# Performance work log

Hardware: AMD Instinct MI355X
Metric: run time of the kernel (lower is better)

Reference implementation:

```python
import jax, jax.numpy as jnp
import numpy as np

EPS = 1e-7  # keras.backend.epsilon()
ROUTINGS = 3


def squash(s, axis=-1):
    # standard capsule squash: ||s||^2/(1+||s||^2) * s/||s||
    n2 = jnp.sum(jnp.square(s), axis=axis, keepdims=True)
    return s * (n2 / (1.0 + n2)) / jnp.sqrt(n2 + EPS)


def setup_inputs() -> dict:
    key = jax.random.key(0)
    k1, k2 = jax.random.split(key)
    B, I, K = 32, 2048, 8          # batch, input capsules, input capsule dim
    J, D = 32, 16                  # output capsules (num_capsules), dim_capsules
    x = jax.random.normal(k1, (B, I, K), dtype=jnp.float32)
    # add_weight with random_normal_initializer(stddev=0.1), shape [J, I, D, K]
    W = 0.1 * jax.random.normal(k2, (J, I, D, K), dtype=jnp.float32)
    return {"x": x, "W": W}


def reference(x, W):
    # u_ji_hat[b,j,i,d] = sum_k W[j,i,d,k] * x[b,i,k]  (the map_fn batched matmul)
    u_hat = jnp.einsum('jidk,bik->bjid', W, x)  # [B, J, I, D]
    B, J, I, D = u_hat.shape
    b = jnp.zeros((B, J, I), dtype=u_hat.dtype)  # routing logits b_ij
    v = None
    for r in range(ROUTINGS):
        c = jax.nn.softmax(b, axis=1)                 # softmax over output capsules J
        s = jnp.einsum('bji,bjid->bjd', c, u_hat)     # weighted sum over input caps i
        v = squash(s, axis=-1)                        # squash over capsule dim (axis=-2 pre-squeeze)
        if r < ROUTINGS - 1:
            # agreement = u_hat^T v : sum over capsule dim d
            b = b + jnp.einsum('bjid,bjd->bji', u_hat, v)
    return v  # [B, J, D] == tf.squeeze(v_j, [2, 4])
```

## Files before the change

kernel.cpp:

```cpp
#include <hip/hip_runtime.h>
#include <hip/hip_fp16.h>


#define ICAP    2048
#define JD      512
#define S_ELEMS 16384
#define EPSQ    1e-7f
#define NBP     256
#define ICH     8

typedef _Float16 h2v __attribute__((ext_vector_type(2)));
union H8 { int4 i4; h2v h[4]; };

#if defined(__has_builtin) && __has_builtin(__builtin_amdgcn_fdot2)
#define FDOT2(a, b, c) __builtin_amdgcn_fdot2((a), (b), (c), false)
#else
__device__ inline float FDOT2(h2v a, h2v b, float c) {
    return c + (float)a[0] * (float)b[0] + (float)a[1] * (float)b[1];
}
#endif
#if defined(__has_builtin) && __has_builtin(__builtin_amdgcn_rcpf)
#define FAST_RCP(x) __builtin_amdgcn_rcpf(x)
#else
#define FAST_RCP(x) (1.0f / (x))
#endif
#if defined(__has_builtin) && __has_builtin(__builtin_amdgcn_rsqf)
#define FAST_RSQ(x) __builtin_amdgcn_rsqf(x)
#else
#define FAST_RSQ(x) rsqrtf(x)
#endif

__global__ __launch_bounds__(256)
void caps_prep(const float4* __restrict__ Wv, const float* __restrict__ x,
               ushort4* __restrict__ Wt, __half* __restrict__ xh) {
    const int i = blockIdx.x;
    const int t = threadIdx.x;
#pragma unroll
    for (int q = 0; q < 4; ++q) {
        const int f  = q * 256 + t;
        const int jj = f >> 5, c = f & 31;
        const float4 w = Wv[(size_t)jj * 65536 + (size_t)i * 32 + c];
        ushort4 h;
        h.x = __half_as_ushort(__float2half(w.x));
        h.y = __half_as_ushort(__float2half(w.y));
        h.z = __half_as_ushort(__float2half(w.z));
        h.w = __half_as_ushort(__float2half(w.w));
        const int dh = c >> 4, cc = (c & 15) >> 1, sub = c & 1;
        Wt[((size_t)i * 512 + cc * 64 + 2 * jj + dh) * 2 + sub] = h;
    }
    const int b = t >> 3, k = t & 7;
    const size_t xi = ((size_t)b * ICAP + i) * 8 + k;
    xh[xi] = __float2half(x[xi]);
}

template <int FIRST>
__global__ __launch_bounds__(512, 1)
void caps_pass(const int4* __restrict__ Wt, const int4* __restrict__ xh,
               const float* __restrict__ vsum, __half* __restrict__ partials) {
    const int tid  = threadIdx.x;
    const int wave = tid >> 6;
    const int lane = tid & 63;
    const int j    = lane & 31;
    const int dh   = lane >> 5;
    const int i0   = blockIdx.x * ICH;

    float vs[4][8], sacc[4][8];
#pragma unroll
    for (int bb = 0; bb < 4; ++bb) {
        const int b = wave + 8 * bb;
        if (!FIRST) {
            const float* vp = vsum + b * JD + j * 16 + dh * 8;
            const float4 a  = *reinterpret_cast<const float4*>(vp);
            const float4 bq = *reinterpret_cast<const float4*>(vp + 4);
            vs[bb][0]=a.x; vs[bb][1]=a.y; vs[bb][2]=a.z; vs[bb][3]=a.w;
            vs[bb][4]=bq.x; vs[bb][5]=bq.y; vs[bb][6]=bq.z; vs[bb][7]=bq.w;
        }
#pragma unroll
        for (int r = 0; r < 8; ++r) sacc[bb][r] = 0.f;
    }

    const int4* wp = Wt + (size_t)i0 * 512 + 2 * j + dh;

#pragma unroll
    for (int il = 0; il < ICH; ++il) {
        H8 w8[8];
#pragma unroll
        for (int cc = 0; cc < 8; ++cc)
            w8[cc].i4 = wp[(size_t)il * 512 + cc * 64];

        const int gi = i0 + il;
#pragma unroll
        for (int bb = 0; bb < 4; ++bb) {
            const int b = wave + 8 * bb;
            H8 xv;
            xv.i4 = xh[(size_t)b * ICAP + gi];

            float u[8], tpart = 0.f;
#pragma unroll
            for (int r = 0; r < 8; ++r) {
                float acc = FDOT2(w8[r].h[0], xv.h[0], 0.f);
                acc = FDOT2(w8[r].h[1], xv.h[1], acc);
                acc = FDOT2(w8[r].h[2], xv.h[2], acc);
                acc = FDOT2(w8[r].h[3], xv.h[3], acc);
                u[r] = acc;
                if (!FIRST) tpart = fmaf(acc, vs[bb][r], tpart);
            }
            float c;
            if (FIRST) {
                c = 0.03125f;
            } else {
                const float t = tpart + __shfl_xor(tpart, 32);
                const float e = __expf(t);
                float se = e;
#pragma unroll
                for (int off = 1; off <= 16; off <<= 1)
                    se += __shfl_xor(se, off);
                c = e * FAST_RCP(se);
            }
#pragma unroll
            for (int r = 0; r < 8; ++r)
                sacc[bb][r] = fmaf(c, u[r], sacc[bb][r]);
        }
    }

    __half* pout = partials + (size_t)blockIdx.x * S_ELEMS;
#pragma unroll
    for (int bb = 0; bb < 4; ++bb) {
        const int b = wave + 8 * bb;
        union { int4 v; __half2 h[4]; } pk;
#pragma unroll
        for (int r = 0; r < 4; ++r)
            pk.h[r] = __floats2half2_rn(sacc[bb][2 * r], sacc[bb][2 * r + 1]);
        *reinterpret_cast<int4*>(pout + b * JD + j * 16 + dh * 8) = pk.v;
    }
}

__global__ __launch_bounds__(1024)
void caps_reduce(const __half* __restrict__ partials, float* __restrict__ vsum,
                 float* __restrict__ out, int first) {
    __shared__ float buf[16][80];
    const int tid = threadIdx.x;
    const int eL  = tid & 63;
    const int sg  = tid >> 6;
    const int e   = blockIdx.x * 64 + eL;

    float s = 0.f;
    const __half* p = partials + (size_t)sg * S_ELEMS + e;
#pragma unroll
    for (int n = 0; n < 16; ++n)
        s += __half2float(p[(size_t)(n * 16) * S_ELEMS]);
    buf[sg][eL] = s;
    __syncthreads();

    if (sg == 0) {
        s = 0.f;
#pragma unroll
        for (int k = 0; k < 16; ++k) s += buf[k][eL];
        float n2 = s * s;
#pragma unroll
        for (int off = 1; off <= 8; off <<= 1)
            n2 += __shfl_xor(n2, off);
        const float scale = n2 * FAST_RCP(1.f + n2) * FAST_RSQ(n2 + EPSQ);
        const float v = s * scale;
        const float old = first ? 0.f : vsum[e];
        vsum[e] = old + v;
        if (out) out[e] = v;
    }
}

extern "C" void kernel_launch(void* const* d_in, const int* in_sizes, int n_in,
                              void* d_out, int out_size, void* d_ws, size_t ws_size,
                              hipStream_t stream) {
    const float* x = (const float*)d_in[0];
    const float* W = (const float*)d_in[1];
    float* out = (float*)d_out;

    ushort4* Wt      = (ushort4*)d_ws;
    __half*  xh      = (__half*)((char*)d_ws + (size_t)ICAP * 512 * 16);
    float*   vsum    = (float*)((char*)xh + (size_t)32 * ICAP * 8 * 2);
    __half*  partials= (__half*)((char*)vsum + S_ELEMS * sizeof(float));

    caps_prep<<<ICAP, 256, 0, stream>>>((const float4*)W, x, Wt, xh);

    caps_pass<1><<<NBP, 512, 0, stream>>>((const int4*)Wt, (const int4*)xh,
                                          vsum, partials);
    caps_reduce<<<S_ELEMS / 64, 1024, 0, stream>>>(partials, vsum, nullptr, 1);

    caps_pass<0><<<NBP, 512, 0, stream>>>((const int4*)Wt, (const int4*)xh,
                                          vsum, partials);
    caps_reduce<<<S_ELEMS / 64, 1024, 0, stream>>>(partials, vsum, nullptr, 0);

    caps_pass<0><<<NBP, 512, 0, stream>>>((const int4*)Wt, (const int4*)xh,
                                          vsum, partials);
    caps_reduce<<<S_ELEMS / 64, 1024, 0, stream>>>(partials, vsum, out, 0);
}
```

Baseline: 161.5 us.

## Fuse prep, routing passes and reductions into one cooperative persistent kernel

Replaces the seven-kernel sequence (prep, three passes, three reductions) with a single cooperative kernel launched over 256 blocks. Each block converts its 8-capsule slice of W and x to fp16 directly into LDS once and reuses it across all three routing iterations. Grid-wide syncs replace the kernel boundaries, and the cross-block reduction plus squash runs inside the same kernel. This removes the global round trip for the transposed fp16 W and the launch gaps, at the cost of grid.sync latency and a large LDS footprint that forces one block per CU. The old multi-kernel path is kept as a fallback if the cooperative launch fails.

```diff
diff --git a/kernel.cpp b/kernel.cpp
--- a/kernel.cpp
+++ b/kernel.cpp
@@ -1,5 +1,8 @@
 #include <hip/hip_runtime.h>
 #include <hip/hip_fp16.h>
+#include <hip/hip_cooperative_groups.h>
+
+namespace cg = cooperative_groups;
 
 
 #define ICAP    2048
@@ -8,6 +11,8 @@
 #define EPSQ    1e-7f
 #define NBP     256
 #define ICH     8
+#define WROW    1040
+#define WIL     (8 * WROW)
 
 typedef _Float16 h2v __attribute__((ext_vector_type(2)));
 union H8 { int4 i4; h2v h[4]; };
@@ -30,6 +35,158 @@
 #define FAST_RSQ(x) rsqrtf(x)
 #endif
 
+__global__ __launch_bounds__(512, 1)
+void caps_fused(const float4* __restrict__ Wv, const float4* __restrict__ Xv,
+                float* __restrict__ vsum, __half* __restrict__ partials,
+                float* __restrict__ out)
+{
+    __shared__ __align__(16) unsigned char sWt[WIL * ICH];
+    __shared__ __align__(16) unsigned char sX[4096];
+    __shared__ float rbuf[8][64];
+
+    const int tid = threadIdx.x;
+    const int bid = blockIdx.x;
+    const int i0  = bid * ICH;
+
+#pragma unroll
+    for (int it = 0; it < 16; ++it) {
+        const int f  = it * 512 + tid;
+        const int q4 = f & 31;
+        const int il = (f >> 5) & 7;
+        const int jj = f >> 8;
+        const float4 w = Wv[((size_t)jj * ICAP + (i0 + il)) * 32 + q4];
+        ushort4 h;
+        h.x = __half_as_ushort(__float2half(w.x));
+        h.y = __half_as_ushort(__float2half(w.y));
+        h.z = __half_as_ushort(__float2half(w.z));
+        h.w = __half_as_ushort(__float2half(w.w));
+        const int d   = q4 >> 1;
+        const int sub = q4 & 1;
+        *reinterpret_cast<ushort4*>(sWt + il * WIL + (d & 7) * WROW
+                                    + (2 * jj + (d >> 3)) * 16 + sub * 8) = h;
+    }
+    {
+        const int k4 = tid & 1, il = (tid >> 1) & 7, b = tid >> 4;
+        const float4 w = Xv[((size_t)b * ICAP + (i0 + il)) * 2 + k4];
+        ushort4 h;
+        h.x = __half_as_ushort(__float2half(w.x));
+        h.y = __half_as_ushort(__float2half(w.y));
+        h.z = __half_as_ushort(__float2half(w.z));
+        h.w = __half_as_ushort(__float2half(w.w));
+        *reinterpret_cast<ushort4*>(sX + (b * 8 + il) * 16 + k4 * 8) = h;
+    }
+    __syncthreads();
+
+    const int wave = tid >> 6, lane = tid & 63;
+    const int j = lane & 31, dh = lane >> 5;
+    float vacc = 0.f;
+
+    cg::grid_group grid = cg::this_grid();
+
+#pragma unroll
+    for (int r = 0; r < 3; ++r) {
+        const bool first = (r == 0);
+        float vs[4][8], sacc[4][8];
+#pragma unroll
+        for (int bb = 0; bb < 4; ++bb) {
+            const int b = wave + 8 * bb;
+            if (!first) {
+                const float* vp = vsum + b * JD + j * 16 + dh * 8;
+                const float4 a  = *reinterpret_cast<const float4*>(vp);
+                const float4 bq = *reinterpret_cast<const float4*>(vp + 4);
+                vs[bb][0]=a.x; vs[bb][1]=a.y; vs[bb][2]=a.z; vs[bb][3]=a.w;
+                vs[bb][4]=bq.x; vs[bb][5]=bq.y; vs[bb][6]=bq.z; vs[bb][7]=bq.w;
+            }
+#pragma unroll
+            for (int q = 0; q < 8; ++q) sacc[bb][q] = 0.f;
+        }
+
+#pragma unroll
+        for (int il = 0; il < ICH; ++il) {
+            H8 w8[8];
+#pragma unroll
+            for (int cc = 0; cc < 8; ++cc)
+                w8[cc].i4 = *reinterpret_cast<const int4*>(
+                    sWt + il * WIL + cc * WROW + (2 * j + dh) * 16);
+#pragma unroll
+            for (int bb = 0; bb < 4; ++bb) {
+                const int b = wave + 8 * bb;
+                H8 xv;
+                xv.i4 = *reinterpret_cast<const int4*>(sX + (b * 8 + il) * 16);
+
+                float u[8], tpart = 0.f;
+#pragma unroll
+                for (int q = 0; q < 8; ++q) {
+                    float acc = FDOT2(w8[q].h[0], xv.h[0], 0.f);
+                    acc = FDOT2(w8[q].h[1], xv.h[1], acc);
+                    acc = FDOT2(w8[q].h[2], xv.h[2], acc);
+                    acc = FDOT2(w8[q].h[3], xv.h[3], acc);
+                    u[q] = acc;
+                    if (!first) tpart = fmaf(acc, vs[bb][q], tpart);
+                }
+                float c;
+                if (first) {
+                    c = 0.03125f;
+                } else {
+                    const float t = tpart + __shfl_xor(tpart, 32);
+                    const float e = __expf(t);
+                    float se = e;
+#pragma unroll
+                    for (int off = 1; off <= 16; off <<= 1)
+                        se += __shfl_xor(se, off);
+                    c = e * FAST_RCP(se);
+                }
+#pragma unroll
+                for (int q = 0; q < 8; ++q)
+                    sacc[bb][q] = fmaf(c, u[q], sacc[bb][q]);
+            }
+        }
+
+        __half* pout = partials + (size_t)bid * S_ELEMS;
+#pragma unroll
+        for (int bb = 0; bb < 4; ++bb) {
+            const int b = wave + 8 * bb;
+            union { int4 v; __half2 h[4]; } pk;
+#pragma unroll
+            for (int q = 0; q < 4; ++q)
+                pk.h[q] = __floats2half2_rn(sacc[bb][2 * q], sacc[bb][2 * q + 1]);
+            *reinterpret_cast<int4*>(pout + b * JD + j * 16 + dh * 8) = pk.v;
+        }
+
+        __threadfence();
+        grid.sync();
+
+        {
+            const int e = bid * 64 + lane;
+            float s = 0.f;
+            const __half* p = partials + (size_t)wave * 32 * S_ELEMS + e;
+#pragma unroll
+            for (int n = 0; n < 32; ++n)
+                s += __half2float(p[(size_t)n * S_ELEMS]);
+            rbuf[wave][lane] = s;
+            __syncthreads();
+            if (wave == 0) {
+                s = 0.f;
+#pragma unroll
+                for (int k = 0; k < 8; ++k) s += rbuf[k][lane];
+                float n2 = s * s;
+#pragma unroll
+                for (int off = 1; off <= 8; off <<= 1)
+                    n2 += __shfl_xor(n2, off);
+                const float scale = n2 * FAST_RCP(1.f + n2) * FAST_RSQ(n2 + EPSQ);
+                const float v = s * scale;
+                if (r == 2) {
+                    out[e] = v;
+                } else {
+                    vacc += v;
+                    vsum[e] = vacc;
+                }
+            }
+        }
+        if (r < 2) { __threadfence(); grid.sync(); }
+    }
+}
+
 __global__ __launch_bounds__(256)
 void caps_prep(const float4* __restrict__ Wv, const float* __restrict__ x,
                ushort4* __restrict__ Wt, __half* __restrict__ xh) {
@@ -76,7 +233,7 @@
             vs[bb][4]=bq.x; vs[bb][5]=bq.y; vs[bb][6]=bq.z; vs[bb][7]=bq.w;
         }
 #pragma unroll
-        for (int r = 0; r < 8; ++r) sacc[bb][r] = 0.f;
+        for (int q = 0; q < 8; ++q) sacc[bb][q] = 0.f;
     }
 
     const int4* wp = Wt + (size_t)i0 * 512 + 2 * j + dh;
@@ -97,13 +254,13 @@
 
             float u[8], tpart = 0.f;
 #pragma unroll
-            for (int r = 0; r < 8; ++r) {
-                float acc = FDOT2(w8[r].h[0], xv.h[0], 0.f);
-                acc = FDOT2(w8[r].h[1], xv.h[1], acc);
-                acc = FDOT2(w8[r].h[2], xv.h[2], acc);
-                acc = FDOT2(w8[r].h[3], xv.h[3], acc);
-                u[r] = acc;
-                if (!FIRST) tpart = fmaf(acc, vs[bb][r], tpart);
+            for (int q = 0; q < 8; ++q) {
+                float acc = FDOT2(w8[q].h[0], xv.h[0], 0.f);
+                acc = FDOT2(w8[q].h[1], xv.h[1], acc);
+                acc = FDOT2(w8[q].h[2], xv.h[2], acc);
+                acc = FDOT2(w8[q].h[3], xv.h[3], acc);
+                u[q] = acc;
+                if (!FIRST) tpart = fmaf(acc, vs[bb][q], tpart);
             }
             float c;
             if (FIRST) {
@@ -118,8 +275,8 @@
                 c = e * FAST_RCP(se);
             }
 #pragma unroll
-            for (int r = 0; r < 8; ++r)
-                sacc[bb][r] = fmaf(c, u[r], sacc[bb][r]);
+            for (int q = 0; q < 8; ++q)
+                sacc[bb][q] = fmaf(c, u[q], sacc[bb][q]);
         }
     }
 
@@ -129,8 +286,8 @@
         const int b = wave + 8 * bb;
         union { int4 v; __half2 h[4]; } pk;
 #pragma unroll
-        for (int r = 0; r < 4; ++r)
-            pk.h[r] = __floats2half2_rn(sacc[bb][2 * r], sacc[bb][2 * r + 1]);
+        for (int q = 0; q < 4; ++q)
+            pk.h[q] = __floats2half2_rn(sacc[bb][2 * q], sacc[bb][2 * q + 1]);
         *reinterpret_cast<int4*>(pout + b * JD + j * 16 + dh * 8) = pk.v;
     }
 }
@@ -175,22 +332,31 @@
     const float* W = (const float*)d_in[1];
     float* out = (float*)d_out;
 
-    ushort4* Wt      = (ushort4*)d_ws;
-    __half*  xh      = (__half*)((char*)d_ws + (size_t)ICAP * 512 * 16);
-    float*   vsum    = (float*)((char*)xh + (size_t)32 * ICAP * 8 * 2);
-    __half*  partials= (__half*)((char*)vsum + S_ELEMS * sizeof(float));
-
-    caps_prep<<<ICAP, 256, 0, stream>>>((const float4*)W, x, Wt, xh);
-
-    caps_pass<1><<<NBP, 512, 0, stream>>>((const int4*)Wt, (const int4*)xh,
-                                          vsum, partials);
-    caps_reduce<<<S_ELEMS / 64, 1024, 0, stream>>>(partials, vsum, nullptr, 1);
-
-    caps_pass<0><<<NBP, 512, 0, stream>>>((const int4*)Wt, (const int4*)xh,
-                                          vsum, partials);
-    caps_reduce<<<S_ELEMS / 64, 1024, 0, stream>>>(partials, vsum, nullptr, 0);
-
-    caps_pass<0><<<NBP, 512, 0, stream>>>((const int4*)Wt, (const int4*)xh,
-                                          vsum, partials);
-    caps_reduce<<<S_ELEMS / 64, 1024, 0, stream>>>(partials, vsum, out, 0);
-}
+    float*   vsum     = (float*)d_ws;
+    __half*  partials = (__half*)((char*)d_ws + 65536);
+    ushort4* Wt       = (ushort4*)((char*)partials + (size_t)NBP * S_ELEMS * 2);
+    __half*  xh       = (__half*)((char*)Wt + (size_t)ICAP * 512 * 16);
+
+    const float4* W4 = (const float4*)W;
+    const float4* x4 = (const float4*)x;
+    void* args[] = {(void*)&W4, (void*)&x4, (void*)&vsum, (void*)&partials,
+                    (void*)&out};
+
+    hipError_t cerr = hipLaunchCooperativeKernel(
+        reinterpret_cast<const void*>(&caps_fused),
+        dim3(NBP), dim3(512), args, 0, stream);
+
+    if (cerr != hipSuccess) {
+        (void)hipGetLastError();
+        caps_prep<<<ICAP, 256, 0, stream>>>((const float4*)W, x, Wt, xh);
+        caps_pass<1><<<NBP, 512, 0, stream>>>((const int4*)Wt, (const int4*)xh,
+                                              vsum, partials);
+        caps_reduce<<<S_ELEMS / 64, 1024, 0, stream>>>(partials, vsum, nullptr, 1);
+        caps_pass<0><<<NBP, 512, 0, stream>>>((const int4*)Wt, (const int4*)xh,
+                                              vsum, partials);
+        caps_reduce<<<S_ELEMS / 64, 1024, 0, stream>>>(partials, vsum, nullptr, 0);
+        caps_pass<0><<<NBP, 512, 0, stream>>>((const int4*)Wt, (const int4*)xh,
+                                              vsum, partials);
+        caps_reduce<<<S_ELEMS / 64, 1024, 0, stream>>>(partials, vsum, out, 0);
+    }
+}
```

New measurement: 523.6 us. 3.24x slower.
